# Performance work log

Hardware: AMD Instinct MI355X
Metric: run time of the kernel (lower is better)

The kernel has to match this reference:

```python
import jax, jax.numpy as jnp
import numpy as np

SCALE = 28.0
ALPHA = 0.6
BETA = 0.4
SCALE_POS = 10.0
SCALE_NEG = 40.0
NUM_CLASSES = 11003
FEATURE_SIZE = 2048
BATCH = 1024


def setup_inputs() -> dict:
    key = jax.random.key(0)
    k1, k2, k3, k4 = jax.random.split(key, 4)
    visual_embed = jax.random.normal(k1, (BATCH, FEATURE_SIZE), dtype=jnp.float32)
    textual_embed = jax.random.normal(k2, (BATCH, FEATURE_SIZE), dtype=jnp.float32)
    labels = jax.random.randint(k3, (BATCH,), 0, NUM_CLASSES, dtype=jnp.int64)
    W = jax.random.normal(k4, (FEATURE_SIZE, NUM_CLASSES), dtype=jnp.float32)
    return {"visual_embed": visual_embed, "textual_embed": textual_embed,
            "labels": labels, "W": W}


def _l2norm(x, axis):
    return x / jnp.linalg.norm(x, axis=axis, keepdims=True)


def _cross_entropy(logits, labels):
    logp = jax.nn.log_softmax(logits, axis=-1)
    return -jnp.take_along_axis(logp, labels[:, None], axis=-1).mean()


def reference(visual_embed, textual_embed, labels, W):
    b = visual_embed.shape[0]
    v = _l2norm(visual_embed, 1)
    t = _l2norm(textual_embed, 1)

    # instance loss: scaled cosine classifier + CE on both modalities
    Wn = _l2norm(W, 0)
    v_logits = SCALE * (v @ Wn)
    t_logits = SCALE * (t @ Wn)
    instance_loss = _cross_entropy(v_logits, labels) + _cross_entropy(t_logits, labels)

    # global align loss: masked soft-margin over full BxB similarity.
    # Original loops rows i and columns i, so every entry is counted twice.
    sim = v @ t.T  # [B, B]
    pos_mask = (labels[:, None] == labels[None, :]).astype(sim.dtype)
    loss_pos = jax.nn.softplus(-SCALE_POS * (sim - ALPHA))
    loss_neg = jax.nn.softplus(SCALE_NEG * (sim - BETA))
    per_pair = pos_mask * loss_pos + (1.0 - pos_mask) * loss_neg
    global_align_loss = 2.0 * per_pair.sum() / b

    return jnp.stack([instance_loss, global_align_loss])
```

## Files before the change

kernel.cpp:

```cpp
#include <hip/hip_runtime.h>
#include <hip/hip_bf16.h>
#include <math.h>

#define BATCH 1024
#define FEAT  2048
#define NCLS  11003
#define NPAD  11008
#define NT1   86
#define NPART (NT1 * 2)
#define M1    2048
#define C_SCALE  28.0f
#define C_ALPHA  0.6f
#define C_BETA   0.4f
#define C_SPOS   10.0f
#define C_SNEG   40.0f
#define XSCALE   16.0f
#define SCL1     (C_SCALE / XSCALE)
#define SIMSCL   (1.0f / (XSCALE * XSCALE))
#define SCALE1   0x7F7F7F7F

typedef float floatx4 __attribute__((ext_vector_type(4)));
typedef float f32x16  __attribute__((ext_vector_type(16)));
typedef int   v8i     __attribute__((ext_vector_type(8)));
typedef unsigned char u8;

#define O_ALIGN  ((size_t)0)
#define O_INST   ((size_t)64)
#define O_FIN    ((size_t)128)
#define O_COLSQ  ((size_t)256)
#define O_XN     ((size_t)44288)
#define O_WT     ((size_t)4238592)
#define O_PSUM   ((size_t)26782976)
#define O_LL     ((size_t)28192000)

#define PREP_WBLOCKS (43 * 32)
#define PREP_TOTAL   (PREP_WBLOCKS + M1)

__device__ inline float softplusf(float x) {
    return (x > 20.f) ? x : log1pf(expf(x));
}

__device__ inline void gll16(const void* g, void* l) {
    __builtin_amdgcn_global_load_lds(
        (const __attribute__((address_space(1))) unsigned int*)g,
        (__attribute__((address_space(3))) unsigned int*)l, 16, 0, 0);
}

__device__ inline unsigned int pack4_fp8(float a, float b, float c, float d) {
    unsigned int p = __builtin_amdgcn_cvt_pk_fp8_f32(a, b, 0, false);
    p = __builtin_amdgcn_cvt_pk_fp8_f32(c, d, p, true);
    return p;
}

__device__ inline int swz(int c) { return c ^ ((c >> 4) & 7); }

__global__ __launch_bounds__(256) void k_prep(const float* __restrict__ vis,
                                              const float* __restrict__ txt,
                                              const float* __restrict__ W,
                                              u8* __restrict__ Xn,
                                              u8* __restrict__ WT,
                                              float* __restrict__ colsq) {
    __shared__ u8 tileT[1024 * 16];
    __shared__ float cps[4][256];
    __shared__ float sb[256];
    int t = threadIdx.x;
    if (blockIdx.x < PREP_WBLOCKS) {
        int c0 = (blockIdx.x % 43) * 256, f0 = (blockIdx.x / 43) * 64;
        int w = t >> 6, l = t & 63;
        int cbase = c0 + 4 * l;
        unsigned int chunks[4][4];
        float ssq0 = 0.f, ssq1 = 0.f, ssq2 = 0.f, ssq3 = 0.f;
        #pragma unroll
        for (int q = 0; q < 4; ++q) {
            float4 row[4];
            #pragma unroll
            for (int rr = 0; rr < 4; ++rr) {
                int f = f0 + w * 16 + q * 4 + rr;
                const float* p = W + (size_t)f * NCLS + cbase;
                float4 v;
                if (cbase + 3 < NCLS) {
                    __builtin_memcpy(&v, p, 16);
                } else {
                    v.x = (cbase + 0 < NCLS) ? p[0] : 0.f;
                    v.y = (cbase + 1 < NCLS) ? p[1] : 0.f;
                    v.z = (cbase + 2 < NCLS) ? p[2] : 0.f;
                    v.w = (cbase + 3 < NCLS) ? p[3] : 0.f;
                }
                row[rr] = v;
            }
            chunks[0][q] = pack4_fp8(row[0].x, row[1].x, row[2].x, row[3].x);
            chunks[1][q] = pack4_fp8(row[0].y, row[1].y, row[2].y, row[3].y);
            chunks[2][q] = pack4_fp8(row[0].z, row[1].z, row[2].z, row[3].z);
            chunks[3][q] = pack4_fp8(row[0].w, row[1].w, row[2].w, row[3].w);
            #pragma unroll
            for (int rr = 0; rr < 4; ++rr) {
                ssq0 += row[rr].x * row[rr].x;
                ssq1 += row[rr].y * row[rr].y;
                ssq2 += row[rr].z * row[rr].z;
                ssq3 += row[rr].w * row[rr].w;
            }
        }
        #pragma unroll
        for (int j = 0; j < 4; ++j) {
            int L = (4 * l + j) * 4 + w;
            int P = L ^ ((L >> 4) & 7);
            *(uint4*)(tileT + P * 16) =
                make_uint4(chunks[j][0], chunks[j][1], chunks[j][2], chunks[j][3]);
        }
        *(float4*)&cps[w][4 * l] = make_float4(ssq0, ssq1, ssq2, ssq3);
        __syncthreads();
        int c = c0 + t;
        uint4 och[4];
        #pragma unroll
        for (int w2 = 0; w2 < 4; ++w2) {
            int L = t * 4 + w2;
            int P = L ^ ((L >> 4) & 7);
            och[w2] = *(const uint4*)(tileT + P * 16);
        }
        uint4* dst = (uint4*)(WT + (size_t)c * FEAT + f0);
        dst[0] = och[0]; dst[1] = och[1]; dst[2] = och[2]; dst[3] = och[3];
        float s = cps[0][t] + cps[1][t] + cps[2][t] + cps[3][t];
        if (c < NCLS) atomicAdd(&colsq[c], s);
    } else {
        int r = blockIdx.x - PREP_WBLOCKS;
        const float* src = (r < BATCH) ? (vis + (size_t)r * FEAT)
                                       : (txt + (size_t)(r - BATCH) * FEAT);
        float4 x0 = ((const float4*)src)[t];
        float4 x1 = ((const float4*)src)[t + 256];
        float ss = x0.x*x0.x + x0.y*x0.y + x0.z*x0.z + x0.w*x0.w
                 + x1.x*x1.x + x1.y*x1.y + x1.z*x1.z + x1.w*x1.w;
        sb[t] = ss; __syncthreads();
        for (int s = 128; s > 0; s >>= 1) { if (t < s) sb[t] += sb[t + s]; __syncthreads(); }
        float rn = rsqrtf(sb[0]) * XSCALE;
        unsigned int* dst = (unsigned int*)(Xn + (size_t)r * FEAT);
        dst[t]       = pack4_fp8(x0.x*rn, x0.y*rn, x0.z*rn, x0.w*rn);
        dst[t + 256] = pack4_fp8(x1.x*rn, x1.y*rn, x1.z*rn, x1.w*rn);
    }
}

__global__ __launch_bounds__(256) void k_gemm(const u8* __restrict__ Xn,
                                              const u8* __restrict__ WT,
                                              const float* __restrict__ colsq,
                                              const int* __restrict__ labels,
                                              float* __restrict__ psum,
                                              float* __restrict__ ll,
                                              float* __restrict__ align_sum) {
    __shared__ u8 As[128 * 64], Bs[128 * 64];
    f32x16 acc[2][2] = {};
    const int t = threadIdx.x;
    const bool is_sim = (blockIdx.y >= NT1);
    int m0, n0;
    const u8 *A, *B;
    if (!is_sim) {
        m0 = blockIdx.x * 128; n0 = blockIdx.y * 128;
        A = Xn; B = WT;
    } else {
        int s = (blockIdx.y - NT1) * 16 + blockIdx.x;
        m0 = (s >> 3) * 128; n0 = (s & 7) * 128;
        A = Xn; B = Xn + (size_t)BATCH * FEAT;
    }
    const int c0s = swz(t), c1s = swz(256 + t);
    const int ra0 = c0s >> 2, h0 = c0s & 3;
    const int ra1 = c1s >> 2, h1 = c1s & 3;
    const u8* Ag0 = A + (size_t)(m0 + ra0) * FEAT + h0 * 16;
    const u8* Ag1 = A + (size_t)(m0 + ra1) * FEAT + h1 * 16;
    const u8* Bg0 = B + (size_t)(n0 + ra0) * FEAT + h0 * 16;
    const u8* Bg1 = B + (size_t)(n0 + ra1) * FEAT + h1 * 16;
    u8* lA0 = As + t * 16;
    u8* lA1 = As + 4096 + t * 16;
    u8* lB0 = Bs + t * 16;
    u8* lB1 = Bs + 4096 + t * 16;

    const int wave = t >> 6, lane = t & 63;
    const int wm = wave >> 1, wn = wave & 1;
    const int l32 = lane & 31, kh = lane >> 5;
    const uint4* Ard[2][2]; const uint4* Brd[2][2];
    #pragma unroll
    for (int i = 0; i < 2; ++i) {
        #pragma unroll
        for (int c = 0; c < 2; ++c) {
            Ard[i][c] = (const uint4*)(As + swz((wm*64 + i*32 + l32)*4 + kh*2 + c) * 16);
            Brd[i][c] = (const uint4*)(Bs + swz((wn*64 + i*32 + l32)*4 + kh*2 + c) * 16);
        }
    }
    for (int kt = 0; kt < FEAT / 64; ++kt) {
        __syncthreads();
        gll16(Ag0, lA0);
        gll16(Ag1, lA1);
        gll16(Bg0, lB0);
        gll16(Bg1, lB1);
        Ag0 += 64; Ag1 += 64; Bg0 += 64; Bg1 += 64;
        __syncthreads();
        v8i a[2], b[2];
        #pragma unroll
        for (int i = 0; i < 2; ++i) {
            ((uint4*)&a[i])[0] = *Ard[i][0];
            ((uint4*)&a[i])[1] = *Ard[i][1];
            ((uint4*)&b[i])[0] = *Brd[i][0];
            ((uint4*)&b[i])[1] = *Brd[i][1];
        }
        #pragma unroll
        for (int i = 0; i < 2; ++i)
            #pragma unroll
            for (int j = 0; j < 2; ++j)
                acc[i][j] = __builtin_amdgcn_mfma_scale_f32_32x32x64_f8f6f4(
                    a[i], b[j], acc[i][j], 0, 0, 0, SCALE1, 0, SCALE1);
    }

    if (!is_sim) {
        float rcol[2]; bool val[2]; int ncol[2];
        #pragma unroll
        for (int j = 0; j < 2; ++j) {
            ncol[j] = n0 + wn*64 + j*32 + l32;
            val[j] = (ncol[j] < NCLS);
            rcol[j] = val[j] ? (SCL1 * rsqrtf(colsq[ncol[j]])) : 0.f;
        }
        const int pidx = blockIdx.y * 2 + wn;
        #pragma unroll
        for (int i = 0; i < 2; ++i) {
            #pragma unroll
            for (int reg = 0; reg < 16; ++reg) {
                int m = m0 + wm*64 + i*32 + (reg & 3) + 8*(reg >> 2) + 4*kh;
                int lm = labels[m & (BATCH - 1)];
                float s = 0.f;
                #pragma unroll
                for (int j = 0; j < 2; ++j) {
                    if (val[j]) {
                        float v = acc[i][j][reg] * rcol[j];
                        if (ncol[j] == lm) ll[m] = v;
                        s += __expf(v - C_SCALE);
                    }
                }
                #pragma unroll
                for (int off = 1; off < 32; off <<= 1) s += __shfl_xor(s, off);
                if (l32 == 0) psum[(size_t)m * NPART + pidx] = s;
            }
        }
    } else {
        int ln[2];
        #pragma unroll
        for (int j = 0; j < 2; ++j) ln[j] = labels[n0 + wn*64 + j*32 + l32];
        float tot = 0.f;
        #pragma unroll
        for (int i = 0; i < 2; ++i) {
            #pragma unroll
            for (int reg = 0; reg < 16; ++reg) {
                int m = m0 + wm*64 + i*32 + (reg & 3) + 8*(reg >> 2) + 4*kh;
                int lm = labels[m];
                #pragma unroll
                for (int j = 0; j < 2; ++j) {
                    float s = acc[i][j][reg] * SIMSCL;
                    float arg = (lm == ln[j]) ? (-C_SPOS * (s - C_ALPHA))
                                              : ( C_SNEG * (s - C_BETA));
                    tot += softplusf(arg);
                }
            }
        }
        #pragma unroll
        for (int off = 1; off < 64; off <<= 1) tot += __shfl_xor(tot, off);
        if (lane == 0) atomicAdd(align_sum, tot);
    }
}

__global__ __launch_bounds__(256) void k_merge(const float* __restrict__ psum,
                                               const float* __restrict__ ll,
                                               float* __restrict__ inst_sum,
                                               const float* __restrict__ align_sum,
                                               int* __restrict__ fin,
                                               float* __restrict__ out) {
    int r = blockIdx.x, t = threadIdx.x;
    float sm = (t < NPART) ? psum[(size_t)r * NPART + t] : 0.f;
    __shared__ float sb[256];
    sb[t] = sm; __syncthreads();
    for (int s = 128; s > 0; s >>= 1) { if (t < s) sb[t] += sb[t+s]; __syncthreads(); }
    if (t == 0) {
        atomicAdd(inst_sum, C_SCALE + logf(sb[0]) - ll[r]);
        __threadfence();
        if (atomicAdd(fin, 1) == M1 - 1) {
            __threadfence();
            float is = atomicAdd(inst_sum, 0.f);
            float as = atomicAdd((float*)align_sum, 0.f);
            out[0] = is / (float)BATCH;
            out[1] = as * 2.f / (float)BATCH;
        }
    }
}

extern "C" void kernel_launch(void* const* d_in, const int* in_sizes, int n_in,
                              void* d_out, int out_size, void* d_ws, size_t ws_size,
                              hipStream_t stream) {
    const float* vis    = (const float*)d_in[0];
    const float* txt    = (const float*)d_in[1];
    const int*   labels = (const int*)  d_in[2];
    const float* W      = (const float*)d_in[3];
    float* out = (float*)d_out;
    char*  ws  = (char*)d_ws;

    float* align_sum = (float*)(ws + O_ALIGN);
    float* inst_sum  = (float*)(ws + O_INST);
    int*   fin       = (int*)  (ws + O_FIN);
    float* colsq     = (float*)(ws + O_COLSQ);
    u8* Xn = (u8*)(ws + O_XN);
    u8* WT = (u8*)(ws + O_WT);
    float* psum = (float*)(ws + O_PSUM);
    float* ll   = (float*)(ws + O_LL);

    hipMemsetAsync(ws, 0, O_XN, stream);

    k_prep <<<dim3(PREP_TOTAL), 256, 0, stream>>>(vis, txt, W, Xn, WT, colsq);
    k_gemm <<<dim3(M1 / 128, NT1 + 4), 256, 0, stream>>>(Xn, WT, colsq, labels,
                                                         psum, ll, align_sum);
    k_merge<<<dim3(M1), 256, 0, stream>>>(psum, ll, inst_sum, align_sum, fin, out);
}
```

Before: 294.6 us.

## Double-buffer LDS tiles in fp8 GEMM to overlap loads with MFMA

Doubles the shared-memory A/B tiles and restructures the K loop into a two-stage ping-pong. The global-to-LDS loads for the next tile are issued before the MFMA work on the current tile. Each stage waits on vmcnt(0) plus a raw barrier instead of two __syncthreads per iteration, so memory latency can hide behind compute. In exchange, LDS use per block doubles, which may lower occupancy.

```diff
diff --git a/kernel.cpp b/kernel.cpp
--- a/kernel.cpp
+++ b/kernel.cpp
@@ -145,7 +145,7 @@
                                               float* __restrict__ psum,
                                               float* __restrict__ ll,
                                               float* __restrict__ align_sum) {
-    __shared__ u8 As[128 * 64], Bs[128 * 64];
+    __shared__ u8 As[2 * 128 * 64], Bs[2 * 128 * 64];
     f32x16 acc[2][2] = {};
     const int t = threadIdx.x;
     const bool is_sim = (blockIdx.y >= NT1);
@@ -183,29 +183,50 @@
             Brd[i][c] = (const uint4*)(Bs + swz((wn*64 + i*32 + l32)*4 + kh*2 + c) * 16);
         }
     }
-    for (int kt = 0; kt < FEAT / 64; ++kt) {
-        __syncthreads();
-        gll16(Ag0, lA0);
-        gll16(Ag1, lA1);
-        gll16(Bg0, lB0);
-        gll16(Bg1, lB1);
-        Ag0 += 64; Ag1 += 64; Bg0 += 64; Bg1 += 64;
-        __syncthreads();
-        v8i a[2], b[2];
-        #pragma unroll
-        for (int i = 0; i < 2; ++i) {
-            ((uint4*)&a[i])[0] = *Ard[i][0];
-            ((uint4*)&a[i])[1] = *Ard[i][1];
-            ((uint4*)&b[i])[0] = *Brd[i][0];
-            ((uint4*)&b[i])[1] = *Brd[i][1];
-        }
-        #pragma unroll
-        for (int i = 0; i < 2; ++i)
-            #pragma unroll
-            for (int j = 0; j < 2; ++j)
-                acc[i][j] = __builtin_amdgcn_mfma_scale_f32_32x32x64_f8f6f4(
-                    a[i], b[j], acc[i][j], 0, 0, 0, SCALE1, 0, SCALE1);
-    }
+
+#define STAGE(buf) do { \
+        gll16(Ag0, lA0 + (buf) * 8192); \
+        gll16(Ag1, lA1 + (buf) * 8192); \
+        gll16(Bg0, lB0 + (buf) * 8192); \
+        gll16(Bg1, lB1 + (buf) * 8192); \
+        Ag0 += 64; Ag1 += 64; Bg0 += 64; Bg1 += 64; \
+    } while (0)
+
+#define WAITB() do { \
+        asm volatile("s_waitcnt vmcnt(0)" ::: "memory"); \
+        __builtin_amdgcn_s_barrier(); \
+        __builtin_amdgcn_sched_barrier(0); \
+    } while (0)
+
+#define COMPUTE(buf) do { \
+        v8i a[2], b[2]; \
+        _Pragma("unroll") \
+        for (int i = 0; i < 2; ++i) { \
+            ((uint4*)&a[i])[0] = *(const uint4*)((const u8*)Ard[i][0] + (buf) * 8192); \
+            ((uint4*)&a[i])[1] = *(const uint4*)((const u8*)Ard[i][1] + (buf) * 8192); \
+            ((uint4*)&b[i])[0] = *(const uint4*)((const u8*)Brd[i][0] + (buf) * 8192); \
+            ((uint4*)&b[i])[1] = *(const uint4*)((const u8*)Brd[i][1] + (buf) * 8192); \
+        } \
+        _Pragma("unroll") \
+        for (int i = 0; i < 2; ++i) \
+            _Pragma("unroll") \
+            for (int j = 0; j < 2; ++j) \
+                acc[i][j] = __builtin_amdgcn_mfma_scale_f32_32x32x64_f8f6f4( \
+                    a[i], b[j], acc[i][j], 0, 0, 0, SCALE1, 0, SCALE1); \
+    } while (0)
+
+    STAGE(0);
+    for (int kt = 0; kt < FEAT / 64; kt += 2) {
+        WAITB();
+        STAGE(1);
+        COMPUTE(0);
+        WAITB();
+        if (kt < FEAT / 64 - 2) STAGE(0);
+        COMPUTE(1);
+    }
+#undef STAGE
+#undef WAITB
+#undef COMPUTE
 
     if (!is_sim) {
         float rcol[2]; bool val[2]; int ncol[2];
```

Result: slower. 368.7 us (+25.1%).
